# Optimization experiments

Measured on AMD Instinct MI355X. Metric: run time of the kernel, lower is better.

## Reference

```python
import jax, jax.numpy as jnp
import numpy as np

B_, L_, H_, P_ = 8, 4096, 512, 256
DT_MIN, DT_MAX = 1e-3, 1e-1


def setup_inputs() -> dict:
    key = jax.random.key(0)
    ks = jax.random.split(key, 6)
    input_sequence = jax.random.normal(ks[0], (B_, L_, H_), jnp.float32)
    # Stable diagonal SSM eigenvalues (HiPPO-like): negative real, spread imaginary
    Lambda_re = -0.5 * jnp.ones((P_,), jnp.float32)
    Lambda_im = jnp.pi * jnp.arange(P_, dtype=jnp.float32)
    # B, C stored as real arrays with trailing real/imag channel, as in the module
    B = jax.random.normal(ks[1], (P_, H_, 2), jnp.float32) / np.sqrt(2.0 * H_)
    C = jax.random.normal(ks[2], (H_, P_, 2), jnp.float32) / np.sqrt(float(P_))
    D = jax.random.normal(ks[3], (H_,), jnp.float32)
    log_step = jax.random.uniform(ks[4], (P_,), jnp.float32,
                                  float(np.log(DT_MIN)), float(np.log(DT_MAX)))
    return dict(input_sequence=input_sequence, Lambda_re=Lambda_re,
                Lambda_im=Lambda_im, B=B, C=C, D=D, log_step=log_step)


def _scan_ssm(Lambda_bar, Bu):
    """Diagonal linear recurrence x_k = Lambda_bar * x_{k-1} + Bu_k via parallel scan.
    Lambda_bar: (P,) complex64; Bu: (L, P) complex64 -> xs: (L, P) complex64."""
    A = jnp.broadcast_to(Lambda_bar, Bu.shape)

    def binop(e_i, e_j):
        a_i, b_i = e_i
        a_j, b_j = e_j
        return a_j * a_i, a_j * b_i + b_j

    _, xs = jax.lax.associative_scan(binop, (A, Bu))
    return xs


def reference(input_sequence, Lambda_re, Lambda_im, B, C, D, log_step):
    # complex parameters (conj_sym=True, clip_eigs=False, zoh discretization)
    Lambda = (Lambda_re + 1j * Lambda_im).astype(jnp.complex64)        # (P,)
    B_tilde = (B[..., 0] + 1j * B[..., 1]).astype(jnp.complex64)       # (P, H)
    C_tilde = (C[..., 0] + 1j * C[..., 1]).astype(jnp.complex64)       # (H, P)
    step = jnp.exp(log_step)                                           # (P,)
    # ZOH: Lambda_bar = exp(Lambda*dt); B_bar = Lambda^{-1}(Lambda_bar - I) B
    Lambda_bar = jnp.exp(Lambda * step)                                # (P,)
    B_bar = ((1.0 / Lambda) * (Lambda_bar - 1.0))[:, None] * B_tilde   # (P, H)
    # project inputs into state space: (B, L, P)
    Bu = jnp.einsum('blh,ph->blp', input_sequence.astype(jnp.complex64), B_bar)
    xs = jax.vmap(lambda bu: _scan_ssm(Lambda_bar, bu))(Bu)            # (B, L, P)
    state = xs[:, -1, :]                                               # (B, P)
    # conj_sym=True -> output uses 2 * Re(C x)
    ys = 2.0 * jnp.einsum('blp,hp->blh', xs, C_tilde).real             # (B, L, H)
    out = ys + D * input_sequence                                      # D-skip
    return out, state
```

## Files before the change

kernel.cpp:

```cpp
#include <hip/hip_runtime.h>
#include <hip/hip_bf16.h>

#define Hh 512
#define Pp 256
#define Ll 4096
#define Bb 8
#define BL (Bb*Ll)
#define Sc 64
#define NC 64

typedef __attribute__((ext_vector_type(8))) __bf16 bf16x8;
typedef __attribute__((ext_vector_type(4))) float  floatx4;

#define LAM_OFF     0
#define LAMS64D_OFF 512
#define B1G_OFF     1024
#define B3G_OFF     (B1G_OFF + 65536)
#define UB16_OFF    (B3G_OFF + 65536)
#define BUB_OFF     (UB16_OFF + 4194304)
#define XSB_OFF     (BUB_OFF + 4194304)
#define AGG_OFF     (XSB_OFF + 4194304)

#define OUT_ELEMS 16777216

#define GLL16(g, l) __builtin_amdgcn_global_load_lds( \
    (const __attribute__((address_space(1))) void*)(g), \
    (__attribute__((address_space(3))) void*)(l), 16, 0, 0)

__device__ __forceinline__ float2 cmul(float2 a, float2 b) {
    return make_float2(a.x*b.x - a.y*b.y, a.x*b.y + a.y*b.x);
}
__device__ __forceinline__ void cfma(float2& acc, float2 a, float2 b) {
    acc.x = fmaf(a.x, b.x, acc.x); acc.x = fmaf(-a.y, b.y, acc.x);
    acc.y = fmaf(a.x, b.y, acc.y); acc.y = fmaf( a.y, b.x, acc.y);
}

__global__ void prep(const float* __restrict__ u,
                     const float* __restrict__ Bmat, const float* __restrict__ Cmat,
                     const float* __restrict__ Lre, const float* __restrict__ Lim,
                     const float* __restrict__ logstep, float2* __restrict__ ws) {
    int bid = blockIdx.x;
    if (bid < 8192) {
        long i = ((long)bid * 256 + threadIdx.x) * 8;
        float4 v0 = *(const float4*)(u + i);
        float4 v1 = *(const float4*)(u + i + 4);
        __align__(16) __hip_bfloat162 t[4];
        t[0] = __float22bfloat162_rn(make_float2(v0.x, v0.y));
        t[1] = __float22bfloat162_rn(make_float2(v0.z, v0.w));
        t[2] = __float22bfloat162_rn(make_float2(v1.x, v1.y));
        t[3] = __float22bfloat162_rn(make_float2(v1.z, v1.w));
        *(bf16x8*)((__hip_bfloat16*)(ws + UB16_OFF) + i) = *(const bf16x8*)t;
    } else if (bid < 8704) {
        int idx = (bid - 8192) * 256 + threadIdx.x;
        int p = idx >> 9, h = idx & 511;
        double lr = (double)Lre[p], li = (double)Lim[p];
        double st = exp((double)logstep[p]);
        double a  = lr * st, th = li * st;
        double er = exp(a);
        double lamr = er * cos(th), lami = er * sin(th);
        double nr = lamr - 1.0, ni = lami;
        double den = lr*lr + li*li;
        float gx = (float)((nr*lr + ni*li)/den), gy = (float)((ni*lr - nr*li)/den);
        float2 b = ((const float2*)Bmat)[idx];
        float re = gx*b.x - gy*b.y;
        float im = gx*b.y + gy*b.x;
        __hip_bfloat16* B1 = (__hip_bfloat16*)(ws + B1G_OFF);
        B1[(2*p)*512 + h]   = __float2bfloat16(re);
        B1[(2*p+1)*512 + h] = __float2bfloat16(im);
    } else if (bid < 9216) {
        int idx = (bid - 8704) * 256 + threadIdx.x;
        int h = idx >> 8, p = idx & 255;
        float2 c = ((const float2*)Cmat)[idx];
        __hip_bfloat162* B3 = (__hip_bfloat162*)(ws + B3G_OFF);
        B3[h*256 + p] = __float22bfloat162_rn(make_float2(2.f*c.x, -2.f*c.y));
    } else {
        int p = threadIdx.x;
        double lr = (double)Lre[p], li = (double)Lim[p];
        double st = exp((double)logstep[p]);
        double a  = lr * st, th = li * st;
        double er = exp(a);
        ws[LAM_OFF + p] = make_float2((float)(er*cos(th)), (float)(er*sin(th)));
        double er64 = exp(64.0 * a), th64 = 64.0 * th;
        ((double2*)(ws + LAMS64D_OFF))[p] = make_double2(er64*cos(th64), er64*sin(th64));
    }
}

template<int EPI>
__global__ void gemm_mfma(const __hip_bfloat16* __restrict__ Ab,
                          const __hip_bfloat16* __restrict__ Bg,
                          void* __restrict__ Cout,
                          const __hip_bfloat16* __restrict__ ub,
                          const float* __restrict__ Dv) {
    __shared__ __align__(16) char lds[16384];
    const int tid = threadIdx.x;
    const int idx = blockIdx.x;
    const int mt  = (idx >> 5) * 8 + (idx & 7);
    const int nt  = (idx >> 3) & 3;
    const long r0 = (long)mt * 128;
    const int  n0 = nt * 128;

    const int rowL = tid >> 2;
    const int seg  = tid & 3;
    const __hip_bfloat16* Asrc = Ab + (r0 + rowL) * 512 + seg * 8;
    const __hip_bfloat16* Bsrc = Bg + (long)(n0 + rowL) * 512 + seg * 8;
    char* ldsA = lds + tid * 16;
    char* ldsB = lds + 8192 + tid * 16;

    const int lane = tid & 63;
    const int quad = lane >> 4;
    const int ml   = lane & 15;
    const int w    = tid >> 6;
    const int wm   = w & 1, wn = w >> 1;

    floatx4 acc[4][4];
    #pragma unroll
    for (int i = 0; i < 4; ++i)
        #pragma unroll
        for (int j = 0; j < 4; ++j) acc[i][j] = (floatx4)0.f;

    for (int kt = 0; kt < 16; ++kt) {
        __syncthreads();
        GLL16(Asrc + kt*32,           ldsA);
        GLL16(Asrc + kt*32 + 64*512,  ldsA + 4096);
        GLL16(Bsrc + kt*32,           ldsB);
        GLL16(Bsrc + kt*32 + 64*512,  ldsB + 4096);
        __syncthreads();

        bf16x8 af[4], bfr[4];
        #pragma unroll
        for (int fm = 0; fm < 4; ++fm)
            af[fm] = *(const bf16x8*)(lds + (wm*64 + fm*16 + ml)*64 + quad*16);
        #pragma unroll
        for (int fn = 0; fn < 4; ++fn)
            bfr[fn] = *(const bf16x8*)(lds + 8192 + (wn*64 + fn*16 + ml)*64 + quad*16);
        #pragma unroll
        for (int fm = 0; fm < 4; ++fm)
            #pragma unroll
            for (int fn = 0; fn < 4; ++fn)
                acc[fm][fn] = __builtin_amdgcn_mfma_f32_16x16x32_bf16(af[fm], bfr[fn], acc[fm][fn], 0, 0, 0);
    }

    #pragma unroll
    for (int fm = 0; fm < 4; ++fm)
        #pragma unroll
        for (int fn = 0; fn < 4; ++fn) {
            int col = n0 + wn*64 + fn*16 + ml;
            float d = (EPI == 1) ? Dv[col] : 0.f;
            #pragma unroll
            for (int reg = 0; reg < 4; ++reg) {
                long row = r0 + wm*64 + fm*16 + quad*4 + reg;
                long o = row * 512 + col;
                if (EPI == 0) {
                    ((__hip_bfloat16*)Cout)[o] = __float2bfloat16(acc[fm][fn][reg]);
                } else {
                    ((float*)Cout)[o] = acc[fm][fn][reg] + d * __bfloat162float(ub[o]);
                }
            }
        }
}

__global__ void k2a(float2* __restrict__ ws) {
    int p = threadIdx.x;
    int bc = blockIdx.x;
    int b = bc >> 6, c = bc & 63;
    float2 lam = ws[LAM_OFF + p];
    float2 lp[8];
    lp[0] = make_float2(1.f, 0.f);
    #pragma unroll
    for (int k = 1; k < 8; ++k) lp[k] = cmul(lp[k-1], lam);
    float2 lam8 = cmul(lp[7], lam);
    const __hip_bfloat162* __restrict__ bub = (const __hip_bfloat162*)(ws + BUB_OFF);
    long base = (long)(b*Ll + c*Sc) * Pp + p;
    float2 agg = make_float2(0.f, 0.f);
    for (int j0 = 0; j0 < Sc; j0 += 8) {
        float2 v[8];
        #pragma unroll
        for (int i = 0; i < 8; ++i)
            v[i] = __bfloat1622float2(bub[base + (long)(j0 + i) * Pp]);
        float2 s0 = make_float2(0.f, 0.f), s1 = make_float2(0.f, 0.f);
        #pragma unroll
        for (int i = 0; i < 8; i += 2) {
            cfma(s0, lp[7 - i], v[i]);
            cfma(s1, lp[6 - i], v[i + 1]);
        }
        float2 G = make_float2(s0.x + s1.x, s0.y + s1.y);
        float2 na = cmul(lam8, agg);
        agg = make_float2(na.x + G.x, na.y + G.y);
    }
    ws[AGG_OFF + bc * Pp + p] = agg;
}

__global__ void k2c(float2* __restrict__ ws, float* __restrict__ dout) {
    int p = threadIdx.x;
    int bc = blockIdx.x;
    int b = bc >> 6, c = bc & 63;
    float2 lam = ws[LAM_OFF + p];
    double2 l64 = ((const double2*)(ws + LAMS64D_OFF))[p];
    double cr = 0.0, ci = 0.0;
    for (int cp = 0; cp < c; ++cp) {
        float2 a = ws[AGG_OFF + (b*NC + cp) * Pp + p];
        double nr = fma(l64.x, cr, (double)a.x); nr = fma(-l64.y, ci, nr);
        double ni = fma(l64.x, ci, (double)a.y); ni = fma( l64.y, cr, ni);
        cr = nr; ci = ni;
    }
    float2 x = make_float2((float)cr, (float)ci);
    const __hip_bfloat162* __restrict__ bub = (const __hip_bfloat162*)(ws + BUB_OFF);
    __hip_bfloat162* __restrict__ xsb = (__hip_bfloat162*)(ws + XSB_OFF);
    long base = (long)(b*Ll + c*Sc) * Pp + p;
    for (int j0 = 0; j0 < Sc; j0 += 8) {
        float2 v[8];
        #pragma unroll
        for (int i = 0; i < 8; ++i)
            v[i] = __bfloat1622float2(bub[base + (long)(j0 + i) * Pp]);
        #pragma unroll
        for (int i = 0; i < 8; ++i) {
            float nr = fmaf(lam.x, x.x, v[i].x); nr = fmaf(-lam.y, x.y, nr);
            float ni = fmaf(lam.x, x.y, v[i].y); ni = fmaf( lam.y, x.x, ni);
            x.x = nr; x.y = ni;
            xsb[base + (long)(j0 + i) * Pp] = __float22bfloat162_rn(make_float2(x.x, x.y));
        }
    }
    if (c == NC - 1) {
        dout[OUT_ELEMS + b * Pp + p] = x.x;
        dout[OUT_ELEMS + Bb * Pp + b * Pp + p] = x.y;
    }
}

extern "C" void kernel_launch(void* const* d_in, const int* in_sizes, int n_in,
                              void* d_out, int out_size, void* d_ws, size_t ws_size,
                              hipStream_t stream) {
    const float* u       = (const float*)d_in[0];
    const float* Lre     = (const float*)d_in[1];
    const float* Lim     = (const float*)d_in[2];
    const float* Bmat    = (const float*)d_in[3];
    const float* Cmat    = (const float*)d_in[4];
    const float* Dv      = (const float*)d_in[5];
    const float* logstep = (const float*)d_in[6];
    float*  out = (float*)d_out;
    float2* ws  = (float2*)d_ws;

    prep<<<9217, 256, 0, stream>>>(u, Bmat, Cmat, Lre, Lim, logstep, ws);

    gemm_mfma<0><<<1024, 256, 0, stream>>>(
        (const __hip_bfloat16*)(ws + UB16_OFF),
        (const __hip_bfloat16*)(ws + B1G_OFF),
        (void*)(ws + BUB_OFF), nullptr, nullptr);

    k2a<<<Bb*NC, 256, 0, stream>>>(ws);
    k2c<<<Bb*NC, 256, 0, stream>>>(ws, out);

    gemm_mfma<1><<<1024, 256, 0, stream>>>(
        (const __hip_bfloat16*)(ws + XSB_OFF),
        (const __hip_bfloat16*)(ws + B3G_OFF),
        (void*)out,
        (const __hip_bfloat16*)(ws + UB16_OFF), Dv);
}
```

Before: 218.6 us.

## Rewrite bf16 GEMMs as 256x256 tiles with double-buffered LDS pipeline

Replaces the 128x128-tile single-buffered MFMA GEMM with a 512-thread kernel that computes 256x256 output tiles. A 64-wide K slice is staged per iteration into two 64KB LDS buffers via global_load_lds, with an XOR-swizzled layout to avoid bank conflicts, and custom vmcnt/lgkmcnt barriers let the next tile's loads overlap the current MFMAs. s_setprio raises wave priority around the MFMA blocks. It trades occupancy and register pressure (128 accumulator floats per thread, 128KB LDS) and a grid of only 256 blocks for more data reuse and overlapped loads.

After: 203.7 us. 1.07x faster.

```diff
diff --git a/kernel.cpp b/kernel.cpp
--- a/kernel.cpp
+++ b/kernel.cpp
@@ -26,6 +26,9 @@
 #define GLL16(g, l) __builtin_amdgcn_global_load_lds( \
     (const __attribute__((address_space(1))) void*)(g), \
     (__attribute__((address_space(3))) void*)(l), 16, 0, 0)
+
+#define BAR_LGKM()  asm volatile("s_waitcnt lgkmcnt(0)\n\ts_barrier" ::: "memory")
+#define BAR_VMN(n)  asm volatile("s_waitcnt vmcnt(" #n ")\n\ts_barrier" ::: "memory")
 
 __device__ __forceinline__ float2 cmul(float2 a, float2 b) {
     return make_float2(a.x*b.x - a.y*b.y, a.x*b.y + a.y*b.x);
@@ -85,71 +88,116 @@
     }
 }
 
+#define STAGE(buf, kt) do { \
+    _Pragma("unroll") \
+    for (int h_ = 0; h_ < 2; ++h_) { \
+        _Pragma("unroll") \
+        for (int r_ = 0; r_ < 2; ++r_) { \
+            GLL16(aSrc + (h_*128 + r_*64)*1024 + (kt)*128, \
+                  ldsSt + (buf)*65536 + h_*16384 + r_*8192); \
+            GLL16(bSrc + (h_*128 + r_*64)*1024 + (kt)*128, \
+                  ldsSt + (buf)*65536 + 32768 + h_*16384 + r_*8192); \
+        } \
+    } \
+} while (0)
+
 template<int EPI>
-__global__ void gemm_mfma(const __hip_bfloat16* __restrict__ Ab,
-                          const __hip_bfloat16* __restrict__ Bg,
-                          void* __restrict__ Cout,
-                          const __hip_bfloat16* __restrict__ ub,
-                          const float* __restrict__ Dv) {
-    __shared__ __align__(16) char lds[16384];
+__global__ __launch_bounds__(512, 2)
+void gemm8(const __hip_bfloat16* __restrict__ A,
+           const __hip_bfloat16* __restrict__ B,
+           void* __restrict__ Cout,
+           const __hip_bfloat16* __restrict__ ub,
+           const float* __restrict__ Dv) {
+    __shared__ __align__(16) char lds[131072];
     const int tid = threadIdx.x;
+    const int w = tid >> 6, l = tid & 63;
+
     const int idx = blockIdx.x;
-    const int mt  = (idx >> 5) * 8 + (idx & 7);
-    const int nt  = (idx >> 3) & 3;
-    const long r0 = (long)mt * 128;
-    const int  n0 = nt * 128;
-
-    const int rowL = tid >> 2;
-    const int seg  = tid & 3;
-    const __hip_bfloat16* Asrc = Ab + (r0 + rowL) * 512 + seg * 8;
-    const __hip_bfloat16* Bsrc = Bg + (long)(n0 + rowL) * 512 + seg * 8;
-    char* ldsA = lds + tid * 16;
-    char* ldsB = lds + 8192 + tid * 16;
-
-    const int lane = tid & 63;
-    const int quad = lane >> 4;
-    const int ml   = lane & 15;
-    const int w    = tid >> 6;
-    const int wm   = w & 1, wn = w >> 1;
-
-    floatx4 acc[4][4];
+    const int swz = (idx & 7) * 32 + (idx >> 3);
+    const int mt = swz >> 1, nt = swz & 1;
+    const long M0 = (long)mt * 256;
+    const int  N0 = nt * 256;
+
+    const int rA  = l >> 3;
+    const int csw = ((l & 7) ^ rA) * 16;
+    const char* aSrc = (const char*)A + (M0 + w*8 + rA) * 1024 + csw;
+    const char* bSrc = (const char*)B + (long)(N0 + w*8 + rA) * 1024 + csw;
+    char* ldsSt = lds + w*1024 + l*16;
+
+    const int quad = l >> 4, ml = l & 15, m7 = ml & 7;
+    const int wm = w & 1, wn = w >> 1;
+    const int o0 = ((quad    ) ^ m7) * 16;
+    const int o1 = ((quad + 4) ^ m7) * 16;
+    const char* aRd = lds + wm*16384 + ml*128;
+    const char* bRd = lds + 32768 + (wn >> 1)*16384 + ((wn & 1)*64 + ml)*128;
+
+    floatx4 acc[8][4];
     #pragma unroll
-    for (int i = 0; i < 4; ++i)
+    for (int i = 0; i < 8; ++i)
         #pragma unroll
         for (int j = 0; j < 4; ++j) acc[i][j] = (floatx4)0.f;
 
-    for (int kt = 0; kt < 16; ++kt) {
-        __syncthreads();
-        GLL16(Asrc + kt*32,           ldsA);
-        GLL16(Asrc + kt*32 + 64*512,  ldsA + 4096);
-        GLL16(Bsrc + kt*32,           ldsB);
-        GLL16(Bsrc + kt*32 + 64*512,  ldsB + 4096);
-        __syncthreads();
-
-        bf16x8 af[4], bfr[4];
-        #pragma unroll
-        for (int fm = 0; fm < 4; ++fm)
-            af[fm] = *(const bf16x8*)(lds + (wm*64 + fm*16 + ml)*64 + quad*16);
-        #pragma unroll
-        for (int fn = 0; fn < 4; ++fn)
-            bfr[fn] = *(const bf16x8*)(lds + 8192 + (wn*64 + fn*16 + ml)*64 + quad*16);
-        #pragma unroll
-        for (int fm = 0; fm < 4; ++fm)
+    STAGE(0, 0);
+    STAGE(1, 1);
+    BAR_VMN(8);
+
+    #pragma unroll
+    for (int t = 0; t < 8; ++t) {
+        const int tb = (t & 1) * 65536;
+
+        {
+            bf16x8 af[8], bfr[4];
+            #pragma unroll
+            for (int fm = 0; fm < 8; ++fm)
+                af[fm] = *(const bf16x8*)(aRd + tb + fm*2048 + o0);
             #pragma unroll
             for (int fn = 0; fn < 4; ++fn)
-                acc[fm][fn] = __builtin_amdgcn_mfma_f32_16x16x32_bf16(af[fm], bfr[fn], acc[fm][fn], 0, 0, 0);
+                bfr[fn] = *(const bf16x8*)(bRd + tb + fn*2048 + o0);
+            __builtin_amdgcn_s_setprio(1);
+            #pragma unroll
+            for (int fm = 0; fm < 8; ++fm)
+                #pragma unroll
+                for (int fn = 0; fn < 4; ++fn)
+                    acc[fm][fn] = __builtin_amdgcn_mfma_f32_16x16x32_bf16(
+                        af[fm], bfr[fn], acc[fm][fn], 0, 0, 0);
+            __builtin_amdgcn_s_setprio(0);
+        }
+
+        {
+            bf16x8 af[8], bfr[4];
+            #pragma unroll
+            for (int fm = 0; fm < 8; ++fm)
+                af[fm] = *(const bf16x8*)(aRd + tb + fm*2048 + o1);
+            #pragma unroll
+            for (int fn = 0; fn < 4; ++fn)
+                bfr[fn] = *(const bf16x8*)(bRd + tb + fn*2048 + o1);
+            BAR_LGKM();
+            if (t + 2 < 8) STAGE(t & 1, t + 2);
+            __builtin_amdgcn_sched_barrier(0);
+            __builtin_amdgcn_s_setprio(1);
+            #pragma unroll
+            for (int fm = 0; fm < 8; ++fm)
+                #pragma unroll
+                for (int fn = 0; fn < 4; ++fn)
+                    acc[fm][fn] = __builtin_amdgcn_mfma_f32_16x16x32_bf16(
+                        af[fm], bfr[fn], acc[fm][fn], 0, 0, 0);
+            __builtin_amdgcn_s_setprio(0);
+        }
+
+        if (t < 6)       BAR_VMN(8);
+        else if (t == 6) BAR_VMN(0);
     }
 
     #pragma unroll
-    for (int fm = 0; fm < 4; ++fm)
+    for (int fm = 0; fm < 8; ++fm)
         #pragma unroll
         for (int fn = 0; fn < 4; ++fn) {
-            int col = n0 + wn*64 + fn*16 + ml;
-            float d = (EPI == 1) ? Dv[col] : 0.f;
+            const int col = N0 + wn*64 + fn*16 + ml;
+            const float d = (EPI == 1) ? Dv[col] : 0.f;
             #pragma unroll
             for (int reg = 0; reg < 4; ++reg) {
-                long row = r0 + wm*64 + fm*16 + quad*4 + reg;
-                long o = row * 512 + col;
+                const long row = M0 + wm*128 + fm*16 + quad*4 + reg;
+                const long o = row * 512 + col;
                 if (EPI == 0) {
                     ((__hip_bfloat16*)Cout)[o] = __float2bfloat16(acc[fm][fn][reg]);
                 } else {
@@ -241,7 +289,7 @@
 
     prep<<<9217, 256, 0, stream>>>(u, Bmat, Cmat, Lre, Lim, logstep, ws);
 
-    gemm_mfma<0><<<1024, 256, 0, stream>>>(
+    gemm8<0><<<256, 512, 0, stream>>>(
         (const __hip_bfloat16*)(ws + UB16_OFF),
         (const __hip_bfloat16*)(ws + B1G_OFF),
         (void*)(ws + BUB_OFF), nullptr, nullptr);
@@ -249,7 +297,7 @@
     k2a<<<Bb*NC, 256, 0, stream>>>(ws);
     k2c<<<Bb*NC, 256, 0, stream>>>(ws, out);
 
-    gemm_mfma<1><<<1024, 256, 0, stream>>>(
+    gemm8<1><<<256, 512, 0, stream>>>(
         (const __hip_bfloat16*)(ws + XSB_OFF),
         (const __hip_bfloat16*)(ws + B3G_OFF),
         (void*)out,
```
